# Optimization experiments

Measured on AMD Instinct MI355X. Metric: run time of the kernel, lower is better.

## Reference

```python
import jax, jax.numpy as jnp
import numpy as np

N, D = 8192, 128

def setup_inputs() -> dict:
    key = jax.random.key(0)
    kF, kS = jax.random.split(key)
    F = jax.random.normal(kF, (N, D), dtype=jnp.float32)
    S = jax.random.uniform(kS, (N, N), dtype=jnp.float32)
    return {"F": F, "S": S, "t": 1, "T": 10}

def reference(F, S, t, T):
    # Pairwise squared euclidean distances via Gram trick:
    # D_ij = ||f_i||^2 + ||f_j||^2 - 2 f_i . f_j  (same math as norm(F[:,None]-F)^2)
    sq = jnp.sum(F * F, axis=1)                      # [N]
    dist2 = sq[:, None] + sq[None, :] - 2.0 * (F @ F.T)  # [N, N]
    # select=False: loss = sum over i of sum_j dist2[i,j] * S[i,j]
    loss = jnp.sum(dist2 * S)
    return loss
```

## Files before the change

### kernel.cpp

```cpp
#include <hip/hip_runtime.h>

#define NN 8192
#define DD 128
#define BI 128
#define BJ 64
#define GX (NN / BJ)
#define GY (NN / BI)
#define NBLK (GX * GY)

typedef __attribute__((ext_vector_type(8))) short bf16x8;
typedef __attribute__((ext_vector_type(4))) float f32x4;

__device__ __forceinline__ ushort f2bf(float x) {
    unsigned u = __float_as_uint(x);
    unsigned r = u + 0x7FFFu + ((u >> 16) & 1u);
    return (ushort)(r >> 16);
}

__device__ __forceinline__ void async16(void* lds, const void* g) {
    __builtin_amdgcn_global_load_lds(
        (const __attribute__((address_space(1))) unsigned*)g,
        (__attribute__((address_space(3))) unsigned*)lds, 16, 0, 0);
}

__global__ void prep_kernel(const float* __restrict__ F, ushort* __restrict__ Fbf,
                            float* __restrict__ sq, int doFbf) {
    int gtid = blockIdx.x * blockDim.x + threadIdx.x;
    int row  = gtid >> 6;
    int lane = threadIdx.x & 63;
    const float2 v = *(const float2*)(F + (size_t)row * DD + lane * 2);
    if (doFbf)
        ((ushort2*)(Fbf + (size_t)row * DD))[lane] = make_ushort2(f2bf(v.x), f2bf(v.y));
    float s = v.x * v.x + v.y * v.y;
    #pragma unroll
    for (int off = 32; off > 0; off >>= 1) s += __shfl_down(s, off);
    if (lane == 0) sq[row] = s;
}

__global__ __launch_bounds__(256, 4) void tile_kernel(
        const ushort* __restrict__ Fbf, const float* __restrict__ S,
        const float* __restrict__ sq, float* __restrict__ partials) {
    __shared__ ushort lI[BI * DD];
    __shared__ float  red[4];

    const int gi  = blockIdx.y * BI;
    const int gj  = blockIdx.x * BJ;
    const int tid = threadIdx.x;
    const int w = tid >> 6, l = tid & 63;
    const int fr = l & 15, g = l >> 4;
    const int jw = w * 16;

    #pragma unroll
    for (int it = 0; it < 8; ++it) {
        const int c   = it * 4 + w;
        const int row = c * 4 + (l >> 4);
        const int src = ((l & 15) * 16) ^ ((row & 7) << 4);
        async16((char*)lI + c * 1024, (const char*)(Fbf + (size_t)(gi + row) * DD) + src);
    }
    __builtin_amdgcn_sched_barrier(0);

    bf16x8 af[4];
    #pragma unroll
    for (int kk = 0; kk < 4; ++kk)
        af[kk] = *(const bf16x8*)(Fbf + (size_t)(gj + jw + fr) * DD + kk * 32 + g * 8);
    float si[8];
    #pragma unroll
    for (int ct = 0; ct < 8; ++ct) si[ct] = sq[gi + ct * 16 + fr];
    const float4 sjv = *(const float4*)(sq + gj + jw + g * 4);
    __builtin_amdgcn_sched_barrier(0);

    f32x4 sv[8];
    const float* sb = S + (size_t)(gi + fr) * NN + gj + jw + g * 4;
    #pragma unroll
    for (int ct = 0; ct < 8; ++ct)
        sv[ct] = *(const f32x4*)(sb + (size_t)ct * 16 * NN);
    __builtin_amdgcn_sched_barrier(0);

    __syncthreads();

    f32x4 acc[8];
    #pragma unroll
    for (int ct = 0; ct < 8; ++ct) acc[ct] = (f32x4){0.f, 0.f, 0.f, 0.f};
    #pragma unroll
    for (int ct = 0; ct < 8; ++ct) {
        const int row = ct * 16 + fr;
        const int sw  = (row & 7) << 4;
        #pragma unroll
        for (int kk = 0; kk < 4; ++kk) {
            const bf16x8 bfr = *(const bf16x8*)((const char*)lI + row * 256 +
                                                ((kk * 64 + g * 16) ^ sw));
            acc[ct] = __builtin_amdgcn_mfma_f32_16x16x32_bf16(af[kk], bfr, acc[ct], 0, 0, 0);
        }
    }

    float part0 = 0.f, part1 = 0.f;
    #pragma unroll
    for (int ct = 0; ct < 8; ++ct) {
        const f32x4 s4 = sv[ct];
        const float sic = si[ct];
        part0 += s4.x * ((sic + sjv.x) - 2.f * acc[ct][0]);
        part1 += s4.y * ((sic + sjv.y) - 2.f * acc[ct][1]);
        part0 += s4.z * ((sic + sjv.z) - 2.f * acc[ct][2]);
        part1 += s4.w * ((sic + sjv.w) - 2.f * acc[ct][3]);
    }
    float part = part0 + part1;

    #pragma unroll
    for (int off = 32; off > 0; off >>= 1) part += __shfl_down(part, off);
    if (l == 0) red[w] = part;
    __syncthreads();
    if (tid == 0)
        partials[blockIdx.y * gridDim.x + blockIdx.x] =
            (red[0] + red[1]) + (red[2] + red[3]);
}

__global__ __launch_bounds__(256, 2) void tile_fb_kernel(
        const float* __restrict__ F, const float* __restrict__ S,
        const float* __restrict__ sq, float* __restrict__ partials) {
    __shared__ ushort lI[BI * DD];
    __shared__ ushort lJ[BI * DD];
    __shared__ float  sqi[BI];
    __shared__ float  sqj[BI];
    __shared__ float  red[4];

    const int gi = blockIdx.y * BI, gj = blockIdx.x * BI;
    const int tid = threadIdx.x;
    const int w = tid >> 6, l = tid & 63;

    const int r0 = tid >> 5;
    const int c4 = (tid & 31) * 4;
    #pragma unroll
    for (int it = 0; it < 16; ++it) {
        const int row = it * 8 + r0;
        const float4 va = *(const float4*)(F + (size_t)(gi + row) * DD + c4);
        const float4 vb = *(const float4*)(F + (size_t)(gj + row) * DD + c4);
        int byte = row * 256 + c4 * 2;
        byte ^= (row & 7) << 4;
        *(ushort4*)((char*)lI + byte) =
            make_ushort4(f2bf(va.x), f2bf(va.y), f2bf(va.z), f2bf(va.w));
        *(ushort4*)((char*)lJ + byte) =
            make_ushort4(f2bf(vb.x), f2bf(vb.y), f2bf(vb.z), f2bf(vb.w));
    }
    if (tid < 128) sqi[tid] = sq[gi + tid];
    else           sqj[tid - 128] = sq[gj + tid - 128];
    __syncthreads();

    const int fr = l & 15;
    const int g  = l >> 4;
    const int jw = w * 32;

    float4 sv0[8], sv1[8];
    #pragma unroll
    for (int ct = 0; ct < 8; ++ct) {
        const float* srow = S + (size_t)(gi + ct * 16 + fr) * NN + gj + jw + g * 4;
        sv0[ct] = *(const float4*)(srow);
        sv1[ct] = *(const float4*)(srow + 16);
    }

    bf16x8 afrag[2][4];
    #pragma unroll
    for (int kk = 0; kk < 4; ++kk) {
        int row = jw + fr;
        int byte = row * 256 + kk * 64 + g * 16; byte ^= (row & 7) << 4;
        afrag[0][kk] = *(const bf16x8*)((const char*)lJ + byte);
        row = jw + 16 + fr;
        byte = row * 256 + kk * 64 + g * 16; byte ^= (row & 7) << 4;
        afrag[1][kk] = *(const bf16x8*)((const char*)lJ + byte);
    }

    f32x4 acc[2][8];
    #pragma unroll
    for (int ct = 0; ct < 8; ++ct) {
        acc[0][ct] = (f32x4){0.f, 0.f, 0.f, 0.f};
        acc[1][ct] = (f32x4){0.f, 0.f, 0.f, 0.f};
    }
    #pragma unroll
    for (int ct = 0; ct < 8; ++ct) {
        #pragma unroll
        for (int kk = 0; kk < 4; ++kk) {
            const int row = ct * 16 + fr;
            int byte = row * 256 + kk * 64 + g * 16; byte ^= (row & 7) << 4;
            const bf16x8 bfrag = *(const bf16x8*)((const char*)lI + byte);
            acc[0][ct] = __builtin_amdgcn_mfma_f32_16x16x32_bf16(afrag[0][kk], bfrag, acc[0][ct], 0, 0, 0);
            acc[1][ct] = __builtin_amdgcn_mfma_f32_16x16x32_bf16(afrag[1][kk], bfrag, acc[1][ct], 0, 0, 0);
        }
    }

    const float4 sj0 = *(const float4*)(sqj + jw + g * 4);
    const float4 sj1 = *(const float4*)(sqj + jw + 16 + g * 4);
    float part = 0.f;
    #pragma unroll
    for (int ct = 0; ct < 8; ++ct) {
        const float sic = sqi[ct * 16 + fr];
        const float4 s0 = sv0[ct], s1 = sv1[ct];
        part += s0.x * (sic + sj0.x - 2.f * acc[0][ct][0]);
        part += s0.y * (sic + sj0.y - 2.f * acc[0][ct][1]);
        part += s0.z * (sic + sj0.z - 2.f * acc[0][ct][2]);
        part += s0.w * (sic + sj0.w - 2.f * acc[0][ct][3]);
        part += s1.x * (sic + sj1.x - 2.f * acc[1][ct][0]);
        part += s1.y * (sic + sj1.y - 2.f * acc[1][ct][1]);
        part += s1.z * (sic + sj1.z - 2.f * acc[1][ct][2]);
        part += s1.w * (sic + sj1.w - 2.f * acc[1][ct][3]);
    }

    #pragma unroll
    for (int off = 32; off > 0; off >>= 1) part += __shfl_down(part, off);
    if (l == 0) red[w] = part;
    __syncthreads();
    if (tid == 0)
        partials[blockIdx.y * gridDim.x + blockIdx.x] = (red[0] + red[1]) + (red[2] + red[3]);
}

__global__ void reduce_kernel(const float* __restrict__ partials, float* __restrict__ out, int n) {
    __shared__ float sm[256];
    const int t = threadIdx.x;
    float s = 0.f;
    for (int i = t; i < n; i += 256) s += partials[i];
    sm[t] = s;
    __syncthreads();
    for (int off = 128; off > 0; off >>= 1) {
        if (t < off) sm[t] += sm[t + off];
        __syncthreads();
    }
    if (t == 0) out[0] = sm[0];
}

extern "C" void kernel_launch(void* const* d_in, const int* in_sizes, int n_in,
                              void* d_out, int out_size, void* d_ws, size_t ws_size,
                              hipStream_t stream) {
    const float* F = (const float*)d_in[0];
    const float* S = (const float*)d_in[1];
    float* sq        = (float*)d_ws;
    float* partials  = sq + NN;
    ushort* Fbf      = (ushort*)((char*)d_ws + 128 * 1024);
    float* out       = (float*)d_out;

    const size_t need = 128 * 1024 + (size_t)NN * DD * 2 + 256;
    const int fast = (ws_size >= need) ? 1 : 0;

    prep_kernel<<<NN / 4, 256, 0, stream>>>(F, Fbf, sq, fast);
    if (fast) {
        tile_kernel<<<dim3(GX, GY), 256, 0, stream>>>(Fbf, S, sq, partials);
        reduce_kernel<<<1, 256, 0, stream>>>(partials, out, NBLK);
    } else {
        tile_fb_kernel<<<dim3(GY, GY), 256, 0, stream>>>(F, S, sq, partials);
        reduce_kernel<<<1, 256, 0, stream>>>(partials, out, GY * GY);
    }
}
```

Before: 79.15 us.

## Make tile kernel persistent over 16 J-tiles with double-buffered async prefetch

Each block now keeps its 128-row I tile in LDS and loops over 16 consecutive 64-column J tiles. The next J tile's bf16 features, S values and squared norms are prefetched into alternating LDS and register buffers, with a vmcnt wait and barrier between iterations. The block grows to 512 threads split across two I halves, and the grid shrinks to 512 blocks, so fewer partials need reducing. This is meant to hide S streaming latency and amortize the I-tile load, at the cost of fewer blocks to fill the GPU and more LDS and registers per block.

New measurement: 94.09 us. 18.9% more time.

```diff
diff --git a/kernel.cpp b/kernel.cpp
--- a/kernel.cpp
+++ b/kernel.cpp
@@ -4,9 +4,10 @@
 #define DD 128
 #define BI 128
 #define BJ 64
-#define GX (NN / BJ)
-#define GY (NN / BI)
-#define NBLK (GX * GY)
+#define NT 16
+#define GXX 8
+#define GYY 64
+#define NBLK (GXX * GYY)
 
 typedef __attribute__((ext_vector_type(8))) short bf16x8;
 typedef __attribute__((ext_vector_type(4))) float f32x4;
@@ -21,6 +22,11 @@
     __builtin_amdgcn_global_load_lds(
         (const __attribute__((address_space(1))) unsigned*)g,
         (__attribute__((address_space(3))) unsigned*)lds, 16, 0, 0);
+}
+__device__ __forceinline__ void async4(void* lds, const void* g) {
+    __builtin_amdgcn_global_load_lds(
+        (const __attribute__((address_space(1))) unsigned*)g,
+        (__attribute__((address_space(3))) unsigned*)lds, 4, 0, 0);
 }
 
 __global__ void prep_kernel(const float* __restrict__ F, ushort* __restrict__ Fbf,
@@ -37,81 +43,135 @@
     if (lane == 0) sq[row] = s;
 }
 
-__global__ __launch_bounds__(256, 4) void tile_kernel(
+#define BODY(T, SVC, SJC, SVN, SJN, RB, WB)                                   \
+  {                                                                           \
+    const int t_ = (T);                                                       \
+    if (t_ < NT - 1) {                                                        \
+      const int gjn = jbase + (t_ + 1) * BJ;                                  \
+      _Pragma("unroll")                                                       \
+      for (int it = 0; it < 2; ++it) {                                        \
+        const int c_ = it * 8 + w;                                            \
+        const int row_ = c_ * 4 + (l >> 4);                                   \
+        const int src_ = ((l & 15) * 16) ^ ((row_ & 7) << 4);                 \
+        async16((char*)(WB) + c_ * 1024,                                      \
+                (const char*)(Fbf + (size_t)(gjn + row_) * DD) + src_);       \
+      }                                                                       \
+      __builtin_amdgcn_sched_barrier(0);                                      \
+      const float* sbn_ = S + (size_t)(gi + ih + fr) * NN + gjn + jw + g * 4; \
+      _Pragma("unroll")                                                       \
+      for (int c = 0; c < 4; ++c)                                             \
+        SVN[c] = *(const f32x4*)(sbn_ + (size_t)c * 16 * NN);                 \
+      SJN = *(const float4*)(sq + gjn + jw + g * 4);                          \
+      __builtin_amdgcn_sched_barrier(0);                                      \
+    }                                                                         \
+    bf16x8 af_[4];                                                            \
+    {                                                                         \
+      const int row_ = jw + fr;                                               \
+      const int sw_ = (row_ & 7) << 4;                                        \
+      _Pragma("unroll")                                                       \
+      for (int kk = 0; kk < 4; ++kk)                                          \
+        af_[kk] = *(const bf16x8*)((const char*)(RB) + row_ * 256 +           \
+                                   ((kk * 64 + g * 16) ^ sw_));               \
+    }                                                                         \
+    f32x4 acc_[4];                                                            \
+    _Pragma("unroll")                                                         \
+    for (int c = 0; c < 4; ++c) acc_[c] = (f32x4){0.f, 0.f, 0.f, 0.f};        \
+    _Pragma("unroll")                                                         \
+    for (int c = 0; c < 4; ++c) {                                             \
+      const int row_ = ih + c * 16 + fr;                                      \
+      const int sw_ = (row_ & 7) << 4;                                        \
+      _Pragma("unroll")                                                       \
+      for (int kk = 0; kk < 4; ++kk) {                                        \
+        const bf16x8 bfr_ = *(const bf16x8*)((const char*)lI + row_ * 256 +   \
+                                             ((kk * 64 + g * 16) ^ sw_));     \
+        acc_[c] = __builtin_amdgcn_mfma_f32_16x16x32_bf16(af_[kk], bfr_,      \
+                                                          acc_[c], 0, 0, 0);  \
+      }                                                                       \
+    }                                                                         \
+    _Pragma("unroll")                                                         \
+    for (int c = 0; c < 4; ++c) {                                             \
+      const float sic_ = sqi[ih + c * 16 + fr];                               \
+      const f32x4 s4_ = SVC[c];                                               \
+      part0 += s4_.x * ((sic_ + SJC.x) - 2.f * acc_[c][0]);                   \
+      part1 += s4_.y * ((sic_ + SJC.y) - 2.f * acc_[c][1]);                   \
+      part0 += s4_.z * ((sic_ + SJC.z) - 2.f * acc_[c][2]);                   \
+      part1 += s4_.w * ((sic_ + SJC.w) - 2.f * acc_[c][3]);                   \
+    }                                                                         \
+    if (t_ < NT - 1) {                                                        \
+      asm volatile("s_waitcnt vmcnt(5)" ::: "memory");                        \
+      __builtin_amdgcn_sched_barrier(0);                                      \
+      __builtin_amdgcn_s_barrier();                                           \
+      __builtin_amdgcn_sched_barrier(0);                                      \
+    }                                                                         \
+  }
+
+__global__ __launch_bounds__(512, 4) void tile_kernel(
         const ushort* __restrict__ Fbf, const float* __restrict__ S,
         const float* __restrict__ sq, float* __restrict__ partials) {
     __shared__ ushort lI[BI * DD];
-    __shared__ float  red[4];
-
-    const int gi  = blockIdx.y * BI;
-    const int gj  = blockIdx.x * BJ;
+    __shared__ ushort lJ0[BJ * DD];
+    __shared__ ushort lJ1[BJ * DD];
+    __shared__ float  sqi[BI];
+    __shared__ float  red[8];
+
+    const int gi    = blockIdx.y * BI;
+    const int jbase = blockIdx.x * (NT * BJ);
     const int tid = threadIdx.x;
     const int w = tid >> 6, l = tid & 63;
     const int fr = l & 15, g = l >> 4;
-    const int jw = w * 16;
-
-    #pragma unroll
-    for (int it = 0; it < 8; ++it) {
-        const int c   = it * 4 + w;
+    const int jw = (w & 3) * 16;
+    const int ih = (w >> 2) * 64;
+
+    #pragma unroll
+    for (int it = 0; it < 4; ++it) {
+        const int c = it * 8 + w;
         const int row = c * 4 + (l >> 4);
         const int src = ((l & 15) * 16) ^ ((row & 7) << 4);
         async16((char*)lI + c * 1024, (const char*)(Fbf + (size_t)(gi + row) * DD) + src);
     }
+    #pragma unroll
+    for (int it = 0; it < 2; ++it) {
+        const int c = it * 8 + w;
+        const int row = c * 4 + (l >> 4);
+        const int src = ((l & 15) * 16) ^ ((row & 7) << 4);
+        async16((char*)lJ0 + c * 1024, (const char*)(Fbf + (size_t)(jbase + row) * DD) + src);
+    }
+    if (w < 2) {
+        float* dstb = sqi + w * 64;
+        async4(dstb, sq + gi + w * 64 + l);
+    }
     __builtin_amdgcn_sched_barrier(0);
 
-    bf16x8 af[4];
-    #pragma unroll
-    for (int kk = 0; kk < 4; ++kk)
-        af[kk] = *(const bf16x8*)(Fbf + (size_t)(gj + jw + fr) * DD + kk * 32 + g * 8);
-    float si[8];
-    #pragma unroll
-    for (int ct = 0; ct < 8; ++ct) si[ct] = sq[gi + ct * 16 + fr];
-    const float4 sjv = *(const float4*)(sq + gj + jw + g * 4);
+    f32x4 svA[4], svB[4];
+    float4 sjA, sjB;
+    {
+        const float* sb0 = S + (size_t)(gi + ih + fr) * NN + jbase + jw + g * 4;
+        #pragma unroll
+        for (int c = 0; c < 4; ++c)
+            svA[c] = *(const f32x4*)(sb0 + (size_t)c * 16 * NN);
+        sjA = *(const float4*)(sq + jbase + jw + g * 4);
+    }
     __builtin_amdgcn_sched_barrier(0);
-
-    f32x4 sv[8];
-    const float* sb = S + (size_t)(gi + fr) * NN + gj + jw + g * 4;
-    #pragma unroll
-    for (int ct = 0; ct < 8; ++ct)
-        sv[ct] = *(const f32x4*)(sb + (size_t)ct * 16 * NN);
+    asm volatile("s_waitcnt vmcnt(5)" ::: "memory");
     __builtin_amdgcn_sched_barrier(0);
-
-    __syncthreads();
-
-    f32x4 acc[8];
-    #pragma unroll
-    for (int ct = 0; ct < 8; ++ct) acc[ct] = (f32x4){0.f, 0.f, 0.f, 0.f};
-    #pragma unroll
-    for (int ct = 0; ct < 8; ++ct) {
-        const int row = ct * 16 + fr;
-        const int sw  = (row & 7) << 4;
-        #pragma unroll
-        for (int kk = 0; kk < 4; ++kk) {
-            const bf16x8 bfr = *(const bf16x8*)((const char*)lI + row * 256 +
-                                                ((kk * 64 + g * 16) ^ sw));
-            acc[ct] = __builtin_amdgcn_mfma_f32_16x16x32_bf16(af[kk], bfr, acc[ct], 0, 0, 0);
-        }
-    }
+    __builtin_amdgcn_s_barrier();
+    __builtin_amdgcn_sched_barrier(0);
 
     float part0 = 0.f, part1 = 0.f;
-    #pragma unroll
-    for (int ct = 0; ct < 8; ++ct) {
-        const f32x4 s4 = sv[ct];
-        const float sic = si[ct];
-        part0 += s4.x * ((sic + sjv.x) - 2.f * acc[ct][0]);
-        part1 += s4.y * ((sic + sjv.y) - 2.f * acc[ct][1]);
-        part0 += s4.z * ((sic + sjv.z) - 2.f * acc[ct][2]);
-        part1 += s4.w * ((sic + sjv.w) - 2.f * acc[ct][3]);
-    }
+    for (int t = 0; t < NT; t += 2) {
+        BODY(t,     svA, sjA, svB, sjB, lJ0, lJ1);
+        BODY(t + 1, svB, sjB, svA, sjA, lJ1, lJ0);
+    }
+
     float part = part0 + part1;
-
     #pragma unroll
     for (int off = 32; off > 0; off >>= 1) part += __shfl_down(part, off);
     if (l == 0) red[w] = part;
     __syncthreads();
     if (tid == 0)
         partials[blockIdx.y * gridDim.x + blockIdx.x] =
-            (red[0] + red[1]) + (red[2] + red[3]);
+            ((red[0] + red[1]) + (red[2] + red[3])) +
+            ((red[4] + red[5]) + (red[6] + red[7]));
 }
 
 __global__ __launch_bounds__(256, 2) void tile_fb_kernel(
@@ -230,20 +290,20 @@
                               hipStream_t stream) {
     const float* F = (const float*)d_in[0];
     const float* S = (const float*)d_in[1];
-    float* sq        = (float*)d_ws;
-    float* partials  = sq + NN;
-    ushort* Fbf      = (ushort*)((char*)d_ws + 128 * 1024);
-    float* out       = (float*)d_out;
-
-    const size_t need = 128 * 1024 + (size_t)NN * DD * 2 + 256;
+    float* sq       = (float*)d_ws;
+    float* partials = sq + NN;
+    ushort* Fbf     = (ushort*)((char*)d_ws + 48 * 1024);
+    float* out      = (float*)d_out;
+
+    const size_t need = 48 * 1024 + (size_t)NN * DD * 2 + 256;
     const int fast = (ws_size >= need) ? 1 : 0;
 
     prep_kernel<<<NN / 4, 256, 0, stream>>>(F, Fbf, sq, fast);
     if (fast) {
-        tile_kernel<<<dim3(GX, GY), 256, 0, stream>>>(Fbf, S, sq, partials);
+        tile_kernel<<<dim3(GXX, GYY), 512, 0, stream>>>(Fbf, S, sq, partials);
         reduce_kernel<<<1, 256, 0, stream>>>(partials, out, NBLK);
     } else {
-        tile_fb_kernel<<<dim3(GY, GY), 256, 0, stream>>>(F, S, sq, partials);
-        reduce_kernel<<<1, 256, 0, stream>>>(partials, out, GY * GY);
-    }
-}
+        tile_fb_kernel<<<dim3(GYY, GYY), 256, 0, stream>>>(F, S, sq, partials);
+        reduce_kernel<<<1, 256, 0, stream>>>(partials, out, GYY * GYY);
+    }
+}
```
